# Kernel tuning notes

Hardware: AMD Instinct MI355X
Metric: run time of the kernel (lower is better)

Reference implementation:

```python
import jax, jax.numpy as jnp
import numpy as np

N_TOKENS = 32768
DIM = 4096
N_EXPERTS = 64
TOPK = 2
UPDATE_BIAS_RATE = 0.001
ROUTE_SCALE = 1.0


def setup_inputs() -> dict:
    key = jax.random.key(0)
    k1, k2 = jax.random.split(key)
    x = jax.random.normal(k1, (N_TOKENS, DIM), dtype=jnp.float32)
    # gate projection weight, as in nn.Parameter(torch.empty(E, dim)) + kaiming init
    weight = jax.random.normal(k2, (N_EXPERTS, DIM), dtype=jnp.float32) * 0.02
    bias = jnp.zeros((N_EXPERTS,), dtype=jnp.float32)          # registered buffer
    target_dist = jnp.full((N_EXPERTS,), 1.0 / N_EXPERTS, dtype=jnp.float32)
    return {"x": x, "weight": weight, "bias": bias, "target_dist": target_dist}


def reference(x, weight, bias, target_dist):
    # scores = linear(nan_to_num(x), W) + bias, softmax in fp32
    xc = jnp.nan_to_num(x, nan=0.0)
    scores = (xc @ weight.T + bias).astype(jnp.float32)        # [N, E]
    probs = jax.nn.softmax(scores, axis=-1)                    # [N, E]
    # top-k: gathered values equal the top-k probabilities
    topv, indices = jax.lax.top_k(probs, TOPK)                 # [N, K], [N, K]
    weights = topv / jnp.sum(topv, axis=-1, keepdims=True)
    weights = weights * ROUTE_SCALE
    # load-balancing stats: bincount with float weights == segment_sum
    expert_weights_sum = jax.ops.segment_sum(
        weights.reshape(-1), indices.reshape(-1), num_segments=N_EXPERTS)
    total_weights = expert_weights_sum.sum()
    load_error = target_dist * total_weights - expert_weights_sum
    new_bias = bias + UPDATE_BIAS_RATE * (load_error / total_weights)
    return weights.astype(x.dtype), indices, new_bias
```

## Files before the change

kernel.cpp:

```cpp
#include <hip/hip_runtime.h>
#include <math.h>

#define N_TOKENS 32768
#define DIM      4096
#define NE       64
#define TM       64
#define BK       64
#define CHUNKS   (DIM / BK)
#define NBLK     (N_TOKENS / TM)
#define EPS_GAP  2e-3f
#define REFINE_BLOCKS 1024

#define WOFF     65664
#define WL_OFF   32896
#define PART_OFF 128
#define WFRAG_ELEMS (512 * 512)

typedef __bf16 bf16x8 __attribute__((ext_vector_type(8)));
typedef float  f32x16 __attribute__((ext_vector_type(16)));

#define SCHED0() __builtin_amdgcn_sched_barrier(0)
#define BAR()    __builtin_amdgcn_s_barrier()

__global__ __launch_bounds__(256) void prep_w(
    const float* __restrict__ w, float* __restrict__ ws)
{
    __bf16* whi = (__bf16*)(ws + WOFF);
    __bf16* wlo = whi + WFRAG_ELEMS;
    const int tid  = blockIdx.x * 256 + threadIdx.x;
    const int f    = tid >> 6, lane = tid & 63;
    const int nt   = f & 1,    K16  = f >> 1;
    const int e    = nt * 32 + (lane & 31);
    const int k    = K16 * 16 + (lane >> 5) * 8;
    const float4 a = *(const float4*)(w + (size_t)e * DIM + k);
    const float4 b = *(const float4*)(w + (size_t)e * DIM + k + 4);
    const float v[8] = {a.x, a.y, a.z, a.w, b.x, b.y, b.z, b.w};
    __bf16 h[8], l[8];
    #pragma unroll
    for (int i = 0; i < 8; ++i) {
        h[i] = (__bf16)v[i];
        l[i] = (__bf16)(v[i] - (float)h[i]);
    }
    *(bf16x8*)(whi + (size_t)tid * 8) = *(bf16x8*)h;
    *(bf16x8*)(wlo + (size_t)tid * 8) = *(bf16x8*)l;
}

__device__ __forceinline__ unsigned pack_pair(float f0, float f1, float& r0, float& r1) {
    const unsigned u0 = __float_as_uint(f0), u1 = __float_as_uint(f1);
    const unsigned h0 = u0 & 0xFFFF0000u,   h1 = u1 & 0xFFFF0000u;
    r0 = f0 - __uint_as_float(h0);
    r1 = f1 - __uint_as_float(h1);
    return (u0 >> 16) | h1;
}
__device__ __forceinline__ void cvt8(const float4 a, const float4 b, uint4& h, uint4& l) {
    float r0, r1, r2, r3, r4, r5, r6, r7;
    h.x = pack_pair(a.x, a.y, r0, r1);
    h.y = pack_pair(a.z, a.w, r2, r3);
    h.z = pack_pair(b.x, b.y, r4, r5);
    h.w = pack_pair(b.z, b.w, r6, r7);
    l.x = (__float_as_uint(r0) >> 16) | (__float_as_uint(r1) & 0xFFFF0000u);
    l.y = (__float_as_uint(r2) >> 16) | (__float_as_uint(r3) & 0xFFFF0000u);
    l.z = (__float_as_uint(r4) >> 16) | (__float_as_uint(r5) & 0xFFFF0000u);
    l.w = (__float_as_uint(r6) >> 16) | (__float_as_uint(r7) & 0xFFFF0000u);
}

__device__ __forceinline__ void gload_lds16(const float* g, float* lds) {
    __builtin_amdgcn_global_load_lds(
        (const __attribute__((address_space(1))) unsigned*)g,
        (__attribute__((address_space(3))) unsigned*)lds, 16, 0, 0);
}

__global__ __launch_bounds__(256) void gate_main(
    const float* __restrict__ x, const float* __restrict__ bias,
    float* __restrict__ out, float* __restrict__ ws)
{
    __shared__ __align__(16) float xs[2][TM * BK];
    __shared__ float sc[TM][68];
    __shared__ float part[NE];
    __shared__ float sbias[NE];

    const __bf16* whi  = (const __bf16*)(ws + WOFF);
    const __bf16* wlo  = whi + WFRAG_ELEMS;
    unsigned* wl_count = (unsigned*)(ws + 64);
    float*    partials = ws + PART_OFF;
    int*      wl       = (int*)(ws + WL_OFF);

    const int t    = threadIdx.x;
    const int lane = t & 63;
    const int wave = t >> 6;
    const int mt   = wave >> 1;
    const int nt   = wave & 1;
    const int tb   = blockIdx.x * TM;
    const int l31  = lane & 31, lhi = lane >> 5;

    if (t < NE) { sbias[t] = bias[t]; part[t] = 0.f; }

    size_t sofs[4];
    int    dofs[4];
    #pragma unroll
    for (int gl = 0; gl < 4; ++gl) {
        const int row  = wave * 16 + gl * 4 + (lane >> 4);
        const int slot = (lane & 15) ^ (row & 15);
        sofs[gl] = (size_t)(tb + row) * DIM + slot * 4;
        dofs[gl] = (wave * 16 + gl * 4) * BK;
    }

    const int a_row = mt * 32 + l31;
    const int abase = a_row * BK;
    const int aswz  = a_row & 15;

    f32x16 acc0, acc12;
    #pragma unroll
    for (int i = 0; i < 16; ++i) { acc0[i] = 0.f; acc12[i] = 0.f; }

    #pragma unroll
    for (int gl = 0; gl < 4; ++gl) gload_lds16(x + sofs[gl],      &xs[0][dofs[gl]]);
    #pragma unroll
    for (int gl = 0; gl < 4; ++gl) gload_lds16(x + sofs[gl] + BK, &xs[1][dofs[gl]]);

    for (int c = 0; c < CHUNKS; ++c) {
        if (c < CHUNKS - 1) { asm volatile("s_waitcnt vmcnt(4)" ::: "memory"); }
        else                { asm volatile("s_waitcnt vmcnt(0)" ::: "memory"); }
        SCHED0(); BAR(); SCHED0();

        const int K16c = c * 4;
        #pragma unroll
        for (int ks = 0; ks < 4; ++ks) {
            const int s0 = ks * 4 + lhi * 2;
            const float4 fa = *(const float4*)&xs[c & 1][abase + ((s0 ^ aswz) << 2)];
            const float4 fb = *(const float4*)&xs[c & 1][abase + (((s0 + 1) ^ aswz) << 2)];
            uint4 h, l;
            cvt8(fa, fb, h, l);
            const size_t bidx = ((size_t)((K16c + ks) * 2 + nt) * 64 + lane) * 8;
            const bf16x8 bh = *(const bf16x8*)(whi + bidx);
            const bf16x8 bl = *(const bf16x8*)(wlo + bidx);
            const bf16x8 ah = __builtin_bit_cast(bf16x8, h);
            const bf16x8 al = __builtin_bit_cast(bf16x8, l);
            acc0  = __builtin_amdgcn_mfma_f32_32x32x16_bf16(ah, bh, acc0,  0, 0, 0);
            acc12 = __builtin_amdgcn_mfma_f32_32x32x16_bf16(al, bh, acc12, 0, 0, 0);
            acc12 = __builtin_amdgcn_mfma_f32_32x32x16_bf16(ah, bl, acc12, 0, 0, 0);
        }

        SCHED0(); BAR(); SCHED0();
        if (c < CHUNKS - 2) {
            const size_t cofs = (size_t)(c + 2) * BK;
            #pragma unroll
            for (int gl = 0; gl < 4; ++gl)
                gload_lds16(x + sofs[gl] + cofs, &xs[c & 1][dofs[gl]]);
        }
    }

    const int e = nt * 32 + l31;
    #pragma unroll
    for (int r = 0; r < 16; ++r) {
        const int tok = mt * 32 + (r & 3) + 8 * (r >> 2) + 4 * lhi;
        sc[tok][e] = acc0[r] + acc12[r];
    }
    __syncthreads();

    if (t < TM) {
        const int tok = t;
        float v1 = -3e38f, v2 = -3e38f, v3 = -3e38f;
        int   i1 = 0,      i2 = 0;
        #pragma unroll 8
        for (int ei = 0; ei < NE; ++ei) {
            const float s = sc[tok][ei] + sbias[ei];
            if (s > v1)      { v3 = v2; v2 = v1; i2 = i1; v1 = s; i1 = ei; }
            else if (s > v2) { v3 = v2; v2 = s;  i2 = ei; }
            else if (s > v3) { v3 = s; }
        }
        const bool risky = (v1 - v2 < EPS_GAP) || (v2 - v3 < EPS_GAP);
        if (risky) {
            const int pos = (int)atomicAdd(wl_count, 1u);
            wl[pos] = tb + tok;
        } else {
            const float ex = expf(v2 - v1);
            const float w1 = 1.f / (1.f + ex);
            const float w2 = ex * w1;
            const size_t g = (size_t)(tb + tok) * 2;
            *(float2*)(out + g)                        = make_float2(w1, w2);
            *(float2*)(out + (size_t)N_TOKENS * 2 + g) = make_float2((float)i1, (float)i2);
            atomicAdd(&part[i1], w1);
            atomicAdd(&part[i2], w2);
        }
    }
    __syncthreads();
    if (t < NE) partials[(size_t)blockIdx.x * NE + t] = part[t];
}

__global__ __launch_bounds__(256) void gate_refine(
    const float* __restrict__ x,
    const float* __restrict__ w,
    const float* __restrict__ bias,
    float* __restrict__ out,
    float* __restrict__ ws)
{
    float*          ews_ref  = ws;
    const unsigned* wl_count = (const unsigned*)(ws + 64);
    const int*      wl       = (const int*)(ws + WL_OFF);

    const int t = threadIdx.x;
    const int e = t >> 2;
    const int q = t & 3;
    __shared__ double sc[NE];

    const unsigned count = *wl_count;
    for (unsigned it = blockIdx.x; it < count; it += gridDim.x) {
        const int tok = wl[it];
        const float* xr = x + (size_t)tok * DIM;
        const float* wr = w + (size_t)e * DIM;
        double s = 0.0;
        const int k0 = q * (DIM / 4), k1 = k0 + DIM / 4;
        for (int k = k0; k < k1; k += 4) {
            const float4 a = *(const float4*)(xr + k);
            const float4 b = *(const float4*)(wr + k);
            s += (double)a.x * (double)b.x;
            s += (double)a.y * (double)b.y;
            s += (double)a.z * (double)b.z;
            s += (double)a.w * (double)b.w;
        }
        s += __shfl_xor(s, 1);
        s += __shfl_xor(s, 2);
        if (q == 0) sc[e] = s + (double)bias[e];
        __syncthreads();

        if (t == 0) {
            double v1 = -1e300, v2 = -1e300;
            int i1 = 0, i2 = 0;
            for (int j = 0; j < NE; ++j) {
                const double sv = sc[j];
                if (sv > v1)      { v2 = v1; i2 = i1; v1 = sv; i1 = j; }
                else if (sv > v2) { v2 = sv; i2 = j; }
            }
            const double ex = exp(v2 - v1);
            const double w1 = 1.0 / (1.0 + ex);
            const double w2 = ex * w1;
            const size_t g = (size_t)tok * 2;
            *(float2*)(out + g)                        = make_float2((float)w1, (float)w2);
            *(float2*)(out + (size_t)N_TOKENS * 2 + g) = make_float2((float)i1, (float)i2);
            atomicAdd(&ews_ref[i1], (float)w1);
            atomicAdd(&ews_ref[i2], (float)w2);
        }
        __syncthreads();
    }
}

__global__ void gate_bias(
    const float* __restrict__ bias,
    const float* __restrict__ target,
    const float* __restrict__ ws,
    float* __restrict__ out)
{
    const int e = threadIdx.x;
    const float* partials = ws + PART_OFF;
    float v = ws[e];
    for (int b = 0; b < NBLK; ++b) v += partials[(size_t)b * NE + e];
    float total = v;
    #pragma unroll
    for (int off = 32; off > 0; off >>= 1)
        total += __shfl_xor(total, off);
    const float nb = bias[e] + 0.001f * ((target[e] * total - v) / total);
    out[(size_t)N_TOKENS * 4 + e] = nb;
}

extern "C" void kernel_launch(void* const* d_in, const int* in_sizes, int n_in,
                              void* d_out, int out_size, void* d_ws, size_t ws_size,
                              hipStream_t stream) {
    const float* x      = (const float*)d_in[0];
    const float* w      = (const float*)d_in[1];
    const float* bias   = (const float*)d_in[2];
    const float* target = (const float*)d_in[3];
    float* out = (float*)d_out;
    float* ws  = (float*)d_ws;

    hipMemsetAsync(ws, 0, 128 * sizeof(float), stream);
    prep_w     <<<128, 256, 0, stream>>>(w, ws);
    gate_main  <<<NBLK, 256, 0, stream>>>(x, bias, out, ws);
    gate_refine<<<REFINE_BLOCKS, 256, 0, stream>>>(x, w, bias, out, ws);
    gate_bias  <<<1, 64, 0, stream>>>(bias, target, ws, out);
}
```

Before: 302.5 us.

## Split K across waves with 32-token tiles and wider 256-column x chunks

The gate GEMM now uses 32-token blocks, so there are twice as many blocks. The four waves split into two expert halves times two K halves, and their partial scores are summed through shared memory. Each x chunk widens to 256 columns, double-buffered with async global-to-LDS loads. Weight hi/lo bf16 fragments are repacked per chunk and loaded into registers before the barrier, which should put more bytes in flight and hide load latency. The final bias kernel spreads the reduction over the now doubled partials across 256 threads. The cost is a larger LDS footprint per block (about 64KB for x), which may lower occupancy.

```diff
diff --git a/kernel.cpp b/kernel.cpp
--- a/kernel.cpp
+++ b/kernel.cpp
@@ -4,45 +4,45 @@
 #define N_TOKENS 32768
 #define DIM      4096
 #define NE       64
-#define TM       64
-#define BK       64
-#define CHUNKS   (DIM / BK)
+#define TM       32
+#define BKF      256
+#define NCH      (DIM / BKF)
 #define NBLK     (N_TOKENS / TM)
 #define EPS_GAP  2e-3f
 #define REFINE_BLOCKS 1024
 
-#define WOFF     65664
-#define WL_OFF   32896
 #define PART_OFF 128
-#define WFRAG_ELEMS (512 * 512)
+#define WL_OFF   65664
+#define WPK_OFF  98432
 
 typedef __bf16 bf16x8 __attribute__((ext_vector_type(8)));
 typedef float  f32x16 __attribute__((ext_vector_type(16)));
 
-#define SCHED0() __builtin_amdgcn_sched_barrier(0)
-#define BAR()    __builtin_amdgcn_s_barrier()
+#define SB0() __builtin_amdgcn_sched_barrier(0)
+#define BAR() __builtin_amdgcn_s_barrier()
 
 __global__ __launch_bounds__(256) void prep_w(
     const float* __restrict__ w, float* __restrict__ ws)
 {
-    __bf16* whi = (__bf16*)(ws + WOFF);
-    __bf16* wlo = whi + WFRAG_ELEMS;
     const int tid  = blockIdx.x * 256 + threadIdx.x;
-    const int f    = tid >> 6, lane = tid & 63;
-    const int nt   = f & 1,    K16  = f >> 1;
+    const int lane = tid & 63;
+    const int j    = (tid >> 6) & 7;
+    const int hl   = (tid >> 9) & 1;
+    const int kh   = (tid >> 10) & 1;
+    const int nt   = (tid >> 11) & 1;
+    const int c    = tid >> 12;
     const int e    = nt * 32 + (lane & 31);
-    const int k    = K16 * 16 + (lane >> 5) * 8;
+    const int k    = (c * 16 + kh * 8 + j) * 16 + (lane >> 5) * 8;
     const float4 a = *(const float4*)(w + (size_t)e * DIM + k);
     const float4 b = *(const float4*)(w + (size_t)e * DIM + k + 4);
     const float v[8] = {a.x, a.y, a.z, a.w, b.x, b.y, b.z, b.w};
-    __bf16 h[8], l[8];
+    __bf16 hv[8], lv[8];
     #pragma unroll
     for (int i = 0; i < 8; ++i) {
-        h[i] = (__bf16)v[i];
-        l[i] = (__bf16)(v[i] - (float)h[i]);
-    }
-    *(bf16x8*)(whi + (size_t)tid * 8) = *(bf16x8*)h;
-    *(bf16x8*)(wlo + (size_t)tid * 8) = *(bf16x8*)l;
+        hv[i] = (__bf16)v[i];
+        lv[i] = (__bf16)(v[i] - (float)hv[i]);
+    }
+    ((bf16x8*)(ws + WPK_OFF))[tid] = hl ? *(bf16x8*)lv : *(bf16x8*)hv;
 }
 
 __device__ __forceinline__ unsigned pack_pair(float f0, float f1, float& r0, float& r1) {
@@ -74,13 +74,12 @@
     const float* __restrict__ x, const float* __restrict__ bias,
     float* __restrict__ out, float* __restrict__ ws)
 {
-    __shared__ __align__(16) float xs[2][TM * BK];
+    __shared__ __align__(16) float xs[2][TM * BKF];
     __shared__ float sc[TM][68];
     __shared__ float part[NE];
     __shared__ float sbias[NE];
 
-    const __bf16* whi  = (const __bf16*)(ws + WOFF);
-    const __bf16* wlo  = whi + WFRAG_ELEMS;
+    const bf16x8* wb   = (const bf16x8*)(ws + WPK_OFF);
     unsigned* wl_count = (unsigned*)(ws + 64);
     float*    partials = ws + PART_OFF;
     int*      wl       = (int*)(ws + WL_OFF);
@@ -88,73 +87,80 @@
     const int t    = threadIdx.x;
     const int lane = t & 63;
     const int wave = t >> 6;
-    const int mt   = wave >> 1;
     const int nt   = wave & 1;
+    const int kh   = wave >> 1;
     const int tb   = blockIdx.x * TM;
     const int l31  = lane & 31, lhi = lane >> 5;
 
     if (t < NE) { sbias[t] = bias[t]; part[t] = 0.f; }
 
-    size_t sofs[4];
-    int    dofs[4];
-    #pragma unroll
-    for (int gl = 0; gl < 4; ++gl) {
-        const int row  = wave * 16 + gl * 4 + (lane >> 4);
-        const int slot = (lane & 15) ^ (row & 15);
-        sofs[gl] = (size_t)(tb + row) * DIM + slot * 4;
-        dofs[gl] = (wave * 16 + gl * 4) * BK;
-    }
-
-    const int a_row = mt * 32 + l31;
-    const int abase = a_row * BK;
-    const int aswz  = a_row & 15;
+    size_t sofs[8];
+    #pragma unroll
+    for (int i = 0; i < 8; ++i) {
+        const int row = wave * 8 + i;
+        sofs[i] = (size_t)(tb + row) * DIM + ((lane ^ (row & 15)) << 2);
+    }
 
     f32x16 acc0, acc12;
     #pragma unroll
     for (int i = 0; i < 16; ++i) { acc0[i] = 0.f; acc12[i] = 0.f; }
 
     #pragma unroll
-    for (int gl = 0; gl < 4; ++gl) gload_lds16(x + sofs[gl],      &xs[0][dofs[gl]]);
-    #pragma unroll
-    for (int gl = 0; gl < 4; ++gl) gload_lds16(x + sofs[gl] + BK, &xs[1][dofs[gl]]);
-
-    for (int c = 0; c < CHUNKS; ++c) {
-        if (c < CHUNKS - 1) { asm volatile("s_waitcnt vmcnt(4)" ::: "memory"); }
-        else                { asm volatile("s_waitcnt vmcnt(0)" ::: "memory"); }
-        SCHED0(); BAR(); SCHED0();
-
-        const int K16c = c * 4;
-        #pragma unroll
-        for (int ks = 0; ks < 4; ++ks) {
-            const int s0 = ks * 4 + lhi * 2;
-            const float4 fa = *(const float4*)&xs[c & 1][abase + ((s0 ^ aswz) << 2)];
-            const float4 fb = *(const float4*)&xs[c & 1][abase + (((s0 + 1) ^ aswz) << 2)];
-            uint4 h, l;
-            cvt8(fa, fb, h, l);
-            const size_t bidx = ((size_t)((K16c + ks) * 2 + nt) * 64 + lane) * 8;
-            const bf16x8 bh = *(const bf16x8*)(whi + bidx);
-            const bf16x8 bl = *(const bf16x8*)(wlo + bidx);
-            const bf16x8 ah = __builtin_bit_cast(bf16x8, h);
-            const bf16x8 al = __builtin_bit_cast(bf16x8, l);
-            acc0  = __builtin_amdgcn_mfma_f32_32x32x16_bf16(ah, bh, acc0,  0, 0, 0);
-            acc12 = __builtin_amdgcn_mfma_f32_32x32x16_bf16(al, bh, acc12, 0, 0, 0);
-            acc12 = __builtin_amdgcn_mfma_f32_32x32x16_bf16(ah, bl, acc12, 0, 0, 0);
-        }
-
-        SCHED0(); BAR(); SCHED0();
-        if (c < CHUNKS - 2) {
-            const size_t cofs = (size_t)(c + 2) * BK;
+    for (int i = 0; i < 8; ++i)
+        gload_lds16(x + sofs[i], &xs[0][(wave * 8 + i) * BKF]);
+    SB0();
+
+    for (int c = 0; c < NCH; ++c) {
+        const int q = c * 4 + nt * 2 + kh;
+        bf16x8 bh[8], bl[8];
+        #pragma unroll
+        for (int j = 0; j < 8; ++j) bh[j] = wb[(q * 2 + 0) * 512 + j * 64 + lane];
+        #pragma unroll
+        for (int j = 0; j < 8; ++j) bl[j] = wb[(q * 2 + 1) * 512 + j * 64 + lane];
+        SB0();
+        if (c + 1 < NCH) {
             #pragma unroll
-            for (int gl = 0; gl < 4; ++gl)
-                gload_lds16(x + sofs[gl] + cofs, &xs[c & 1][dofs[gl]]);
-        }
+            for (int i = 0; i < 8; ++i)
+                gload_lds16(x + sofs[i] + (size_t)(c + 1) * BKF,
+                            &xs[(c + 1) & 1][(wave * 8 + i) * BKF]);
+        }
+        SB0();
+        if (c + 1 < NCH) { asm volatile("s_waitcnt vmcnt(8)" ::: "memory"); }
+        else             { asm volatile("s_waitcnt vmcnt(0)" ::: "memory"); }
+        SB0(); BAR(); SB0();
+
+        const float* buf = xs[c & 1];
+        #pragma unroll
+        for (int j = 0; j < 8; ++j) {
+            const int s0 = (kh * 8 + j) * 4 + lhi * 2;
+            const float4 fa = *(const float4*)&buf[l31 * BKF + ((s0 ^ (l31 & 15)) << 2)];
+            const float4 fb = *(const float4*)&buf[l31 * BKF + (((s0 + 1) ^ (l31 & 15)) << 2)];
+            uint4 hh, ll;
+            cvt8(fa, fb, hh, ll);
+            const bf16x8 ah = __builtin_bit_cast(bf16x8, hh);
+            const bf16x8 al = __builtin_bit_cast(bf16x8, ll);
+            acc0  = __builtin_amdgcn_mfma_f32_32x32x16_bf16(ah, bh[j], acc0,  0, 0, 0);
+            acc12 = __builtin_amdgcn_mfma_f32_32x32x16_bf16(al, bh[j], acc12, 0, 0, 0);
+            acc12 = __builtin_amdgcn_mfma_f32_32x32x16_bf16(ah, bl[j], acc12, 0, 0, 0);
+        }
+        SB0(); BAR(); SB0();
     }
 
     const int e = nt * 32 + l31;
-    #pragma unroll
-    for (int r = 0; r < 16; ++r) {
-        const int tok = mt * 32 + (r & 3) + 8 * (r >> 2) + 4 * lhi;
-        sc[tok][e] = acc0[r] + acc12[r];
+    if (kh == 0) {
+        #pragma unroll
+        for (int r = 0; r < 16; ++r) {
+            const int tok = (r & 3) + 8 * (r >> 2) + 4 * lhi;
+            sc[tok][e] = acc0[r] + acc12[r];
+        }
+    }
+    __syncthreads();
+    if (kh == 1) {
+        #pragma unroll
+        for (int r = 0; r < 16; ++r) {
+            const int tok = (r & 3) + 8 * (r >> 2) + 4 * lhi;
+            sc[tok][e] += acc0[r] + acc12[r];
+        }
     }
     __syncthreads();
 
@@ -245,22 +251,30 @@
     }
 }
 
-__global__ void gate_bias(
+__global__ __launch_bounds__(256) void gate_bias(
     const float* __restrict__ bias,
     const float* __restrict__ target,
     const float* __restrict__ ws,
     float* __restrict__ out)
 {
-    const int e = threadIdx.x;
+    __shared__ float red[4][NE];
+    const int t = threadIdx.x;
+    const int e = t & 63, seg = t >> 6;
     const float* partials = ws + PART_OFF;
-    float v = ws[e];
-    for (int b = 0; b < NBLK; ++b) v += partials[(size_t)b * NE + e];
-    float total = v;
-    #pragma unroll
-    for (int off = 32; off > 0; off >>= 1)
-        total += __shfl_xor(total, off);
-    const float nb = bias[e] + 0.001f * ((target[e] * total - v) / total);
-    out[(size_t)N_TOKENS * 4 + e] = nb;
+    float v = 0.f;
+    for (int b = seg * 256; b < seg * 256 + 256; ++b)
+        v += partials[(size_t)b * NE + e];
+    red[seg][e] = v;
+    __syncthreads();
+    if (t < NE) {
+        const float vv = red[0][t] + red[1][t] + red[2][t] + red[3][t] + ws[t];
+        float total = vv;
+        #pragma unroll
+        for (int off = 32; off > 0; off >>= 1)
+            total += __shfl_xor(total, off);
+        const float nb = bias[t] + 0.001f * ((target[t] * total - vv) / total);
+        out[(size_t)N_TOKENS * 4 + t] = nb;
+    }
 }
 
 extern "C" void kernel_launch(void* const* d_in, const int* in_sizes, int n_in,
@@ -274,8 +288,8 @@
     float* ws  = (float*)d_ws;
 
     hipMemsetAsync(ws, 0, 128 * sizeof(float), stream);
-    prep_w     <<<128, 256, 0, stream>>>(w, ws);
+    prep_w     <<<256, 256, 0, stream>>>(w, ws);
     gate_main  <<<NBLK, 256, 0, stream>>>(x, bias, out, ws);
     gate_refine<<<REFINE_BLOCKS, 256, 0, stream>>>(x, w, bias, out, ws);
-    gate_bias  <<<1, 64, 0, stream>>>(bias, target, ws, out);
-}
+    gate_bias  <<<1, 256, 0, stream>>>(bias, target, ws, out);
+}
```

After: 303.8 us. No clear change (+0.4%).
